# Kernel tuning notes

Hardware: AMD Instinct MI355X
Metric: run time of the kernel (lower is better)

## Reference

```python
import jax, jax.numpy as jnp
import numpy as np

N_NODES = 50000
N_EDGES = 800000
N_GRAPHS = 512
IN_CH = 64
HID = 64
NEG_SLOPE = 0.2  # PyG GATConv default


def leaky_relu(x):
    return jnp.where(x >= 0, x, NEG_SLOPE * x)


def gat_conv(x, src, dst, W, a_src, a_dst, bias):
    # x: [N, in]; src/dst: [E] (self-loops already included)
    h = x @ W                                   # [N, hid]
    # per-edge attention logits (heads=1)
    alpha_s = h @ a_src                         # [N]
    alpha_d = h @ a_dst                         # [N]
    logits = leaky_relu(alpha_s[src] + alpha_d[dst])   # [E]
    # segment softmax over destination nodes
    seg_max = jax.ops.segment_max(logits, dst, num_segments=N_NODES)
    seg_max = jnp.where(jnp.isfinite(seg_max), seg_max, 0.0)
    ex = jnp.exp(logits - seg_max[dst])
    denom = jax.ops.segment_sum(ex, dst, num_segments=N_NODES)
    alpha = ex / jnp.maximum(denom[dst], 1e-16)
    # scatter-weighted aggregation of source features
    out = jax.ops.segment_sum(alpha[:, None] * h[src], dst, num_segments=N_NODES)
    return out + bias


def setup_inputs() -> dict:
    key = jax.random.key(0)
    ks = jax.random.split(key, 12)
    x = jax.random.normal(ks[0], (N_NODES, IN_CH), dtype=jnp.float32)
    edge_index = jax.random.randint(ks[1], (2, N_EDGES), 0, N_NODES, dtype=jnp.int64)
    batch = jnp.sort(jax.random.randint(ks[2], (N_NODES,), 0, N_GRAPHS, dtype=jnp.int64))
    s1 = 1.0 / np.sqrt(IN_CH)
    s2 = 1.0 / np.sqrt(HID)
    W1 = jax.random.normal(ks[3], (IN_CH, HID), dtype=jnp.float32) * s1
    a_src1 = jax.random.normal(ks[4], (HID,), dtype=jnp.float32) * s2
    a_dst1 = jax.random.normal(ks[5], (HID,), dtype=jnp.float32) * s2
    b1 = jnp.zeros((HID,), dtype=jnp.float32)
    W2 = jax.random.normal(ks[6], (HID, HID), dtype=jnp.float32) * s2
    a_src2 = jax.random.normal(ks[7], (HID,), dtype=jnp.float32) * s2
    a_dst2 = jax.random.normal(ks[8], (HID,), dtype=jnp.float32) * s2
    b2 = jnp.zeros((HID,), dtype=jnp.float32)
    return {"x": x, "edge_index": edge_index, "batch": batch,
            "W1": W1, "a_src1": a_src1, "a_dst1": a_dst1, "b1": b1,
            "W2": W2, "a_src2": a_src2, "a_dst2": a_dst2, "b2": b2}


def reference(x, edge_index, batch, W1, a_src1, a_dst1, b1, W2, a_src2, a_dst2, b2):
    # add self-loops (PyG GATConv default add_self_loops=True)
    loops = jnp.arange(N_NODES, dtype=edge_index.dtype)
    src = jnp.concatenate([edge_index[0], loops])
    dst = jnp.concatenate([edge_index[1], loops])
    h = jax.nn.elu(gat_conv(x, src, dst, W1, a_src1, a_dst1, b1))
    h = jax.nn.elu(gat_conv(h, src, dst, W2, a_src2, a_dst2, b2))
    # global mean pool per graph
    sums = jax.ops.segment_sum(h, batch, num_segments=N_GRAPHS)        # [G, hid]
    cnt = jax.ops.segment_sum(jnp.ones((N_NODES,), h.dtype), batch, num_segments=N_GRAPHS)
    return sums / jnp.maximum(cnt, 1.0)[:, None]
```

## Files before the change

### kernel.cpp

```cpp
#include <hip/hip_runtime.h>
#include <hip/hip_bf16.h>
#include <math.h>

#define N_NODES_C 50000
#define N_EDGES_C 800000
#define E_TOT_C   (N_EDGES_C + N_NODES_C)
#define N_GRAPHS_C 512
#define CH 64
#define NBUCK 391
#define NB_BUCK 256
#define BCAP 3328
#define TRF_NODES 64
#define NB_TRF ((N_NODES_C + TRF_NODES - 1) / TRF_NODES)
#define FAT_NODES 32
#define NB_FAT ((N_NODES_C + FAT_NODES - 1) / FAT_NODES)

__device__ __forceinline__ float wave_reduce_sum(float v) {
#pragma unroll
    for (int m = 32; m >= 1; m >>= 1) v += __shfl_xor(v, m, 64);
    return v;
}

__device__ __forceinline__ void fma8(float wv, uint4 u, float* a) {
    a[0] = fmaf(wv, __uint_as_float(u.x << 16), a[0]);
    a[1] = fmaf(wv, __uint_as_float(u.x & 0xFFFF0000u), a[1]);
    a[2] = fmaf(wv, __uint_as_float(u.y << 16), a[2]);
    a[3] = fmaf(wv, __uint_as_float(u.y & 0xFFFF0000u), a[3]);
    a[4] = fmaf(wv, __uint_as_float(u.z << 16), a[4]);
    a[5] = fmaf(wv, __uint_as_float(u.z & 0xFFFF0000u), a[5]);
    a[6] = fmaf(wv, __uint_as_float(u.w << 16), a[6]);
    a[7] = fmaf(wv, __uint_as_float(u.w & 0xFFFF0000u), a[7]);
}


__device__ __forceinline__ float agg_node_value(
    int n, int lane, const __hip_bfloat16* __restrict__ h,
    const float* __restrict__ as, const float* __restrict__ ad,
    const float* __restrict__ bias,
    const unsigned int* __restrict__ row_ptr,
    const unsigned short* __restrict__ csr_src, int& ch_out)
{
    unsigned rp = row_ptr[n];
    float adn = ad[n];
    int beg = (int)(rp >> 8);
    int deg = (int)(rp & 255u);
    int sub = lane >> 3;
    int cg  = (lane & 7) << 3;
    int ch  = cg | sub;
    ch_out = ch;
    if (deg <= 32) {
        int dm = deg - 1;
        int sA = (int)csr_src[beg + min(sub, dm)];
        int sB = (int)csr_src[beg + min(sub + 8, dm)];
        uint4 u0 = *reinterpret_cast<const uint4*>(h + (size_t)sA * CH + cg);
        uint4 u1 = *reinterpret_cast<const uint4*>(h + (size_t)sB * CH + cg);
        bool two = (deg > 16);
        uint4 u2 = make_uint4(0, 0, 0, 0), u3 = make_uint4(0, 0, 0, 0);
        if (two) {
            int sC = (int)csr_src[beg + min(sub + 16, dm)];
            int sD = (int)csr_src[beg + min(sub + 24, dm)];
            u2 = *reinterpret_cast<const uint4*>(h + (size_t)sC * CH + cg);
            u3 = *reinterpret_cast<const uint4*>(h + (size_t)sD * CH + cg);
        }
        int s_reg = (int)csr_src[beg + min(lane, dm)];
        float v0 = as[s_reg] + adn;
        v0 = (v0 >= 0.f) ? v0 : 0.2f * v0;
        float ex = (lane < deg) ? __expf(v0) : 0.f;
        float w0 = __shfl(ex, sub, 64);
        float w1 = __shfl(ex, sub + 8, 64);
        float ssum = wave_reduce_sum(ex);
        float a[8] = {0.f, 0.f, 0.f, 0.f, 0.f, 0.f, 0.f, 0.f};
        fma8(w0, u0, a); fma8(w1, u1, a);
        if (two) {
            float w2 = __shfl(ex, sub + 16, 64);
            float w3 = __shfl(ex, sub + 24, 64);
            fma8(w2, u2, a); fma8(w3, u3, a);
        }
        float inv = 1.f / fmaxf(ssum, 1e-16f);
        bool hi5 = (lane & 32) != 0;
        float t0 = __shfl_xor(hi5 ? a[0] : a[4], 32, 64);
        float t1 = __shfl_xor(hi5 ? a[1] : a[5], 32, 64);
        float t2 = __shfl_xor(hi5 ? a[2] : a[6], 32, 64);
        float t3 = __shfl_xor(hi5 ? a[3] : a[7], 32, 64);
        float b0 = (hi5 ? a[4] : a[0]) + t0;
        float b1 = (hi5 ? a[5] : a[1]) + t1;
        float b2 = (hi5 ? a[6] : a[2]) + t2;
        float b3 = (hi5 ? a[7] : a[3]) + t3;
        bool hi4 = (lane & 16) != 0;
        float u0s = __shfl_xor(hi4 ? b0 : b2, 16, 64);
        float u1s = __shfl_xor(hi4 ? b1 : b3, 16, 64);
        float c0 = (hi4 ? b2 : b0) + u0s;
        float c1 = (hi4 ? b3 : b1) + u1s;
        bool hi3 = (lane & 8) != 0;
        float v1 = __shfl_xor(hi3 ? c0 : c1, 8, 64);
        float r  = (hi3 ? c1 : c0) + v1;
        float v = r * inv + bias[ch];
        return (v > 0.f) ? v : __expf(v) - 1.f;
    } else if (deg <= 64) {
        int s_reg = (int)csr_src[beg + min(lane, deg - 1)];
        float ex = 0.f;
        if (lane < deg) {
            float v = as[s_reg] + adn;
            v = (v >= 0.f) ? v : 0.2f * v;
            ex = __expf(v);
        }
        float ssum = wave_reduce_sum(ex);
        float inv = 1.f / fmaxf(ssum, 1e-16f);
        float a[8] = {0.f, 0.f, 0.f, 0.f, 0.f, 0.f, 0.f, 0.f};
        int full = deg >> 4, rem = deg & 15;
        for (int j = 0; j < full; ++j) {
            int e1 = j * 16 + sub;
            int e2 = e1 + 8;
            int   s1 = __shfl(s_reg, e1, 64);
            int   s2 = __shfl(s_reg, e2, 64);
            float w1 = __shfl(ex, e1, 64);
            float w2 = __shfl(ex, e2, 64);
            uint4 u1 = *reinterpret_cast<const uint4*>(h + (size_t)s1 * CH + cg);
            uint4 u2 = *reinterpret_cast<const uint4*>(h + (size_t)s2 * CH + cg);
            fma8(w1, u1, a); fma8(w2, u2, a);
        }
        if (rem) {
            int dm = deg - 1;
            int e1 = full * 16 + sub;
            int   s1 = __shfl(s_reg, min(e1, dm), 64);
            float w1 = __shfl(ex, e1, 64);
            uint4 u1 = *reinterpret_cast<const uint4*>(h + (size_t)s1 * CH + cg);
            fma8(w1, u1, a);
            if (rem > 8) {
                int e2 = e1 + 8;
                int   s2 = __shfl(s_reg, min(e2, dm), 64);
                float w2 = __shfl(ex, e2, 64);
                uint4 u2 = *reinterpret_cast<const uint4*>(h + (size_t)s2 * CH + cg);
                fma8(w2, u2, a);
            }
        }
        bool hi5 = (lane & 32) != 0;
        float t0 = __shfl_xor(hi5 ? a[0] : a[4], 32, 64);
        float t1 = __shfl_xor(hi5 ? a[1] : a[5], 32, 64);
        float t2 = __shfl_xor(hi5 ? a[2] : a[6], 32, 64);
        float t3 = __shfl_xor(hi5 ? a[3] : a[7], 32, 64);
        float b0 = (hi5 ? a[4] : a[0]) + t0;
        float b1 = (hi5 ? a[5] : a[1]) + t1;
        float b2 = (hi5 ? a[6] : a[2]) + t2;
        float b3 = (hi5 ? a[7] : a[3]) + t3;
        bool hi4 = (lane & 16) != 0;
        float u0s = __shfl_xor(hi4 ? b0 : b2, 16, 64);
        float u1s = __shfl_xor(hi4 ? b1 : b3, 16, 64);
        float c0 = (hi4 ? b2 : b0) + u0s;
        float c1 = (hi4 ? b3 : b1) + u1s;
        bool hi3 = (lane & 8) != 0;
        float v1 = __shfl_xor(hi3 ? c0 : c1, 8, 64);
        float r  = (hi3 ? c1 : c0) + v1;
        float v = r * inv + bias[ch];
        return (v > 0.f) ? v : __expf(v) - 1.f;
    } else {
        ch_out = lane;
        int end = beg + deg;
        float ssum = 0.f;
        for (int i = beg + lane; i < end; i += 64) {
            float v = as[csr_src[i]] + adn;
            v = (v >= 0.f) ? v : 0.2f * v;
            ssum += __expf(v);
        }
        ssum = wave_reduce_sum(ssum);
        float inv = 1.f / fmaxf(ssum, 1e-16f);
        float acc = 0.f;
        for (int i = beg; i < end; ++i) {
            int s = csr_src[i];
            float v = as[s] + adn;
            v = (v >= 0.f) ? v : 0.2f * v;
            float ww = __expf(v);
            acc = fmaf(ww, __bfloat162float(h[(size_t)s * CH + lane]), acc);
        }
        acc = acc * inv + bias[lane];
        return (acc > 0.f) ? acc : __expf(acc) - 1.f;
    }
}


struct __align__(16) TrfSmem {
    __align__(16) float Wl[64][68];
    __align__(16) float xs[64][68];
    float wsv[64], wdv[64];
};
struct BuildSmem { int cnt[NBUCK]; int lbase[NBUCK]; };
union __align__(16) FusedSmem { TrfSmem t; BuildSmem b; };


__device__ __forceinline__ void build_body(
    BuildSmem& sm, int blk, const int* __restrict__ ei,
    int* __restrict__ bucket_cnt, unsigned int* __restrict__ buck_edges)
{
    int t = threadIdx.x;
    for (int i = t; i < NBUCK; i += 256) sm.cnt[i] = 0;
    __syncthreads();
    const int CHUNK = (E_TOT_C + NB_BUCK - 1) / NB_BUCK;
    int beg = blk * CHUNK, end = min(beg + CHUNK, E_TOT_C);
    for (int e = beg + t; e < end; e += 256) {
        int d = (e < N_EDGES_C) ? ei[N_EDGES_C + e] : (e - N_EDGES_C);
        atomicAdd(&sm.cnt[d >> 7], 1);
    }
    __syncthreads();
    for (int b = t; b < NBUCK; b += 256) {
        int c = sm.cnt[b];
        sm.lbase[b] = (c > 0) ? atomicAdd(&bucket_cnt[b], c) : 0;
        sm.cnt[b] = 0;
    }
    __syncthreads();
    for (int e = beg + t; e < end; e += 256) {
        int s_, d_;
        if (e < N_EDGES_C) { s_ = ei[e]; d_ = ei[N_EDGES_C + e]; }
        else               { s_ = d_ = e - N_EDGES_C; }
        int b = d_ >> 7;
        int pos = sm.lbase[b] + atomicAdd(&sm.cnt[b], 1);
        buck_edges[b * BCAP + pos] = ((unsigned)(d_ & 127) << 16) | (unsigned)s_;
    }
}


__device__ __forceinline__ void transform_body(
    TrfSmem& sm, int bb,
    const float* __restrict__ xin, const float* __restrict__ W,
    const float* __restrict__ a_s, const float* __restrict__ a_d,
    __hip_bfloat16* __restrict__ hout, float* __restrict__ as_out,
    float* __restrict__ ad_out)
{
    int t = threadIdx.x;
    const float4* W4 = (const float4*)W;
    for (int i = t; i < 1024; i += 256) {
        int row = i >> 4, f4 = i & 15;
        *reinterpret_cast<float4*>(&sm.Wl[row][f4 * 4]) = W4[i];
    }
    int n0 = bb * TRF_NODES;
    int nn = min(TRF_NODES, N_NODES_C - n0);
    if (nn < TRF_NODES) {
        for (int idx = t; idx < 64 * TRF_NODES; idx += 256) {
            int k = idx >> 6, row = idx & 63;
            if (row >= nn) sm.xs[k][row] = 0.f;
        }
    }
    for (int idx = t; idx < nn * 16; idx += 256) {
        int row = idx >> 4, f4 = idx & 15;
        float4 v = *reinterpret_cast<const float4*>(xin + (size_t)(n0 + row) * CH + f4 * 4);
        sm.xs[f4 * 4 + 0][row] = v.x;
        sm.xs[f4 * 4 + 1][row] = v.y;
        sm.xs[f4 * 4 + 2][row] = v.z;
        sm.xs[f4 * 4 + 3][row] = v.w;
    }
    __syncthreads();
    if (t < 64) {
        float ss = 0.f, dd = 0.f;
#pragma unroll 8
        for (int c2 = 0; c2 < 64; ++c2) {
            float wv = sm.Wl[t][c2];
            ss = fmaf(wv, a_s[c2], ss);
            dd = fmaf(wv, a_d[c2], dd);
        }
        sm.wsv[t] = ss; sm.wdv[t] = dd;
    }
    int w = t >> 6, c = t & 63, lane = t & 63;
    int r0 = w * 16;
    float acc[16];
#pragma unroll
    for (int i = 0; i < 16; ++i) acc[i] = 0.f;
#pragma unroll 8
    for (int k = 0; k < 64; ++k) {
        float wl = sm.Wl[k][c];
        const float4* xp = reinterpret_cast<const float4*>(&sm.xs[k][r0]);
        float4 xa = xp[0], xb = xp[1], xc = xp[2], xd = xp[3];
        acc[0]  = fmaf(xa.x, wl, acc[0]);  acc[1]  = fmaf(xa.y, wl, acc[1]);
        acc[2]  = fmaf(xa.z, wl, acc[2]);  acc[3]  = fmaf(xa.w, wl, acc[3]);
        acc[4]  = fmaf(xb.x, wl, acc[4]);  acc[5]  = fmaf(xb.y, wl, acc[5]);
        acc[6]  = fmaf(xb.z, wl, acc[6]);  acc[7]  = fmaf(xb.w, wl, acc[7]);
        acc[8]  = fmaf(xc.x, wl, acc[8]);  acc[9]  = fmaf(xc.y, wl, acc[9]);
        acc[10] = fmaf(xc.z, wl, acc[10]); acc[11] = fmaf(xc.w, wl, acc[11]);
        acc[12] = fmaf(xd.x, wl, acc[12]); acc[13] = fmaf(xd.y, wl, acc[13]);
        acc[14] = fmaf(xd.z, wl, acc[14]); acc[15] = fmaf(xd.w, wl, acc[15]);
    }
    size_t hb = (size_t)(n0 + r0) * CH + c;
#pragma unroll
    for (int i = 0; i < 16; ++i)
        if (r0 + i < nn) hout[hb + (size_t)i * CH] = __float2bfloat16(acc[i]);
    __syncthreads();
    int kb = lane & 3;
    int rloc = r0 + (lane >> 2);
    float ps = 0.f, pd = 0.f;
#pragma unroll
    for (int j = 0; j < 16; ++j) {
        int k = kb + 4 * j;
        float xv = sm.xs[k][rloc];
        ps = fmaf(xv, sm.wsv[k], ps);
        pd = fmaf(xv, sm.wdv[k], pd);
    }
    ps += __shfl_xor(ps, 1, 64); ps += __shfl_xor(ps, 2, 64);
    pd += __shfl_xor(pd, 1, 64); pd += __shfl_xor(pd, 2, 64);
    if (kb == 0 && rloc < nn) {
        as_out[n0 + rloc] = ps;
        ad_out[n0 + rloc] = pd;
    }
}


__global__ __launch_bounds__(256) void fused_build_trf(
    const int* __restrict__ ei, int* __restrict__ bucket_cnt,
    unsigned int* __restrict__ buck_edges,
    const float* __restrict__ xin, const float* __restrict__ W,
    const float* __restrict__ a_s, const float* __restrict__ a_d,
    __hip_bfloat16* __restrict__ hout, float* __restrict__ as_out,
    float* __restrict__ ad_out)
{
    __shared__ FusedSmem sm;
    if (blockIdx.x < NB_BUCK)
        build_body(sm.b, blockIdx.x, ei, bucket_cnt, buck_edges);
    else
        transform_body(sm.t, blockIdx.x - NB_BUCK, xin, W, a_s, a_d, hout, as_out, ad_out);
}


__global__ __launch_bounds__(512) void bucket_to_csr(const unsigned int* __restrict__ buck_edges,
                                                     const int* __restrict__ bucket_cnt,
                                                     const int* __restrict__ batch,
                                                     unsigned short* __restrict__ csr_src,
                                                     unsigned int* __restrict__ row_ptr,
                                                     int* __restrict__ gstart) {
    __shared__ unsigned int ebuf[BCAP];
    __shared__ unsigned short sbuf[BCAP];
    __shared__ int deg[128], off[128], cur[128];
    __shared__ int wsum;
    int bb = blockIdx.x, t = threadIdx.x;
    if (bb < 196 && t < 256) {
        int i = bb * 256 + t;
        if (i < N_NODES_C) {
            int bcur = batch[i];
            int bprev = (i > 0) ? batch[i - 1] : -1;
            for (int g = bprev + 1; g <= bcur; ++g) gstart[g] = i;
            if (i == N_NODES_C - 1)
                for (int g = bcur + 1; g <= N_GRAPHS_C; ++g) gstart[g] = N_NODES_C;
        }
    }
    int base = bb * BCAP;
    int size = min(bucket_cnt[bb], BCAP);
    int node0 = bb << 7;
    int nnodes = min(128, N_NODES_C - node0);
    for (int i = t; i < size; i += 512) ebuf[i] = buck_edges[base + i];
    if (t < 128) deg[t] = 0;
    __syncthreads();
    for (int i = t; i < size; i += 512) atomicAdd(&deg[(ebuf[i] >> 16) & 127], 1);
    __syncthreads();
    int myscan = 0;
    if (t < 128) {
        int l = t & 63;
        int s = deg[t];
#pragma unroll
        for (int o = 1; o < 64; o <<= 1) {
            int u = __shfl_up(s, o, 64);
            if (l >= o) s += u;
        }
        myscan = s;
        if (t == 63) wsum = s;
    }
    __syncthreads();
    if (t < 128) {
        int add = (t >= 64) ? wsum : 0;
        off[t] = myscan + add - deg[t];
        cur[t] = 0;
    }
    __syncthreads();
    for (int i = t; i < size; i += 512) {
        unsigned pk = ebuf[i];
        int l = (pk >> 16) & 127;
        int p = atomicAdd(&cur[l], 1);
        sbuf[off[l] + p] = (unsigned short)(pk & 0xFFFFu);
    }
    __syncthreads();
    for (int i = t; i < size; i += 512) csr_src[base + i] = sbuf[i];
    if (t < nnodes)
        row_ptr[node0 + t] = ((unsigned)(base + off[t]) << 8) | (unsigned)min(deg[t], 255);
}


struct __align__(16) FatSmem {
    __align__(16) float Wl[64][68];
    __align__(16) float xs[64][36];
    float wsv[64], wdv[64];
};

__global__ __launch_bounds__(512) void fused_agg_trf(
    const __hip_bfloat16* __restrict__ h1, const float* __restrict__ as1n,
    const float* __restrict__ ad1n, const float* __restrict__ b1,
    const unsigned int* __restrict__ row_ptr, const unsigned short* __restrict__ csr_src,
    const float* __restrict__ W2, const float* __restrict__ a_s2,
    const float* __restrict__ a_d2,
    __hip_bfloat16* __restrict__ hout2, float* __restrict__ as_out2,
    float* __restrict__ ad_out2)
{
    __shared__ FatSmem sm;
    int t = threadIdx.x, bb = blockIdx.x;
    int wv = t >> 6, lane = t & 63;
    int n0 = bb * FAT_NODES;
    int nn = min(FAT_NODES, N_NODES_C - n0);
    const float4* W4 = (const float4*)W2;
    for (int i = t; i < 1024; i += 512) {
        int row = i >> 4, f4 = i & 15;
        *reinterpret_cast<float4*>(&sm.Wl[row][f4 * 4]) = W4[i];
    }
    if (nn < FAT_NODES) {
        for (int idx = t; idx < 64 * FAT_NODES; idx += 512) {
            int k = idx >> 5, row = idx & 31;
            if (row >= nn) sm.xs[k][row] = 0.f;
        }
    }
    for (int q = 0; q < 4; ++q) {
        int nl = wv * 4 + q;
        if (nl < nn) {
            int ch;
            float v = agg_node_value(n0 + nl, lane, h1, as1n, ad1n, b1,
                                     row_ptr, csr_src, ch);
            sm.xs[ch][nl] = v;
        }
    }
    __syncthreads();
    if (t < 64) {
        float ss = 0.f, dd = 0.f;
#pragma unroll 8
        for (int c2 = 0; c2 < 64; ++c2) {
            float wv2 = sm.Wl[t][c2];
            ss = fmaf(wv2, a_s2[c2], ss);
            dd = fmaf(wv2, a_d2[c2], dd);
        }
        sm.wsv[t] = ss; sm.wdv[t] = dd;
    }
    int c = lane;
    int r0 = wv * 4;
    float acc[4] = {0.f, 0.f, 0.f, 0.f};
#pragma unroll 8
    for (int k = 0; k < 64; ++k) {
        float wl = sm.Wl[k][c];
        float4 xa = *reinterpret_cast<const float4*>(&sm.xs[k][r0]);
        acc[0] = fmaf(xa.x, wl, acc[0]);
        acc[1] = fmaf(xa.y, wl, acc[1]);
        acc[2] = fmaf(xa.z, wl, acc[2]);
        acc[3] = fmaf(xa.w, wl, acc[3]);
    }
    size_t hb = (size_t)(n0 + r0) * CH + c;
#pragma unroll
    for (int i = 0; i < 4; ++i)
        if (r0 + i < nn) hout2[hb + (size_t)i * CH] = __float2bfloat16(acc[i]);
    __syncthreads();
    int kb = lane & 15;
    int rloc = r0 + (lane >> 4);
    float ps = 0.f, pd = 0.f;
#pragma unroll
    for (int j = 0; j < 4; ++j) {
        int k = kb + 16 * j;
        float xv = sm.xs[k][rloc];
        ps = fmaf(xv, sm.wsv[k], ps);
        pd = fmaf(xv, sm.wdv[k], pd);
    }
    ps += __shfl_xor(ps, 1, 64); ps += __shfl_xor(ps, 2, 64);
    ps += __shfl_xor(ps, 4, 64); ps += __shfl_xor(ps, 8, 64);
    pd += __shfl_xor(pd, 1, 64); pd += __shfl_xor(pd, 2, 64);
    pd += __shfl_xor(pd, 4, 64); pd += __shfl_xor(pd, 8, 64);
    if (kb == 0 && rloc < nn) {
        as_out2[n0 + rloc] = ps;
        ad_out2[n0 + rloc] = pd;
    }
}


__global__ __launch_bounds__(256) void agg_pool(
    const __hip_bfloat16* __restrict__ h2, const float* __restrict__ as2n,
    const float* __restrict__ ad2n, const float* __restrict__ b2,
    const unsigned int* __restrict__ row_ptr, const unsigned short* __restrict__ csr_src,
    const int* __restrict__ batch, const int* __restrict__ gstart,
    float* __restrict__ out)
{
    int t = threadIdx.x;
    int w = t >> 6, lane = t & 63;
    int n = blockIdx.x * 4 + w;
    int ch;
    float v = agg_node_value(n, lane, h2, as2n, ad2n, b2, row_ptr, csr_src, ch);
    int g = batch[n];
    float cnt = (float)(gstart[g + 1] - gstart[g]);
    atomicAdd(&out[g * CH + ch], v / fmaxf(cnt, 1.f));
}


extern "C" void kernel_launch(void* const* d_in, const int* in_sizes, int n_in,
                              void* d_out, int out_size, void* d_ws, size_t ws_size,
                              hipStream_t stream)
{
    const float* x   = (const float*)d_in[0];
    const int*   ei  = (const int*)d_in[1];
    const int*   bat = (const int*)d_in[2];
    const float* W1  = (const float*)d_in[3];
    const float* as1 = (const float*)d_in[4];
    const float* ad1 = (const float*)d_in[5];
    const float* b1  = (const float*)d_in[6];
    const float* W2  = (const float*)d_in[7];
    const float* as2 = (const float*)d_in[8];
    const float* ad2 = (const float*)d_in[9];
    const float* b2  = (const float*)d_in[10];
    float* out = (float*)d_out;

    char* ws = (char*)d_ws;
    size_t off = 0;
    auto alloc = [&](size_t bytes) -> void* {
        void* p = ws + off;
        off += (bytes + 255) & ~size_t(255);
        return p;
    };
    __hip_bfloat16* hbuf1 = (__hip_bfloat16*)alloc(sizeof(__hip_bfloat16) * N_NODES_C * CH);
    __hip_bfloat16* hbuf2 = (__hip_bfloat16*)alloc(sizeof(__hip_bfloat16) * N_NODES_C * CH);
    float* as1n = (float*)alloc(sizeof(float) * N_NODES_C);
    float* ad1n = (float*)alloc(sizeof(float) * N_NODES_C);
    float* as2n = (float*)alloc(sizeof(float) * N_NODES_C);
    float* ad2n = (float*)alloc(sizeof(float) * N_NODES_C);
    int*   bucket_cnt = (int*)alloc(sizeof(int) * NBUCK);
    unsigned int* buck_edges = (unsigned int*)alloc(sizeof(unsigned) * NBUCK * BCAP);
    unsigned short* csr_src  = (unsigned short*)alloc(sizeof(unsigned short) * NBUCK * BCAP);
    unsigned int* row_ptr    = (unsigned int*)alloc(sizeof(unsigned) * N_NODES_C);
    int*   gstart  = (int*)alloc(sizeof(int) * (N_GRAPHS_C + 1));

    const int NB_AGG = N_NODES_C / 4;

    hipMemsetAsync(bucket_cnt, 0, sizeof(int) * NBUCK, stream);
    hipMemsetAsync(out, 0, sizeof(float) * N_GRAPHS_C * CH, stream);

    fused_build_trf<<<NB_BUCK + NB_TRF, 256, 0, stream>>>(ei, bucket_cnt, buck_edges,
                                                          x, W1, as1, ad1,
                                                          hbuf1, as1n, ad1n);
    bucket_to_csr<<<NBUCK, 512, 0, stream>>>(buck_edges, bucket_cnt, bat,
                                             csr_src, row_ptr, gstart);
    fused_agg_trf<<<NB_FAT, 512, 0, stream>>>(hbuf1, as1n, ad1n, b1,
                                              row_ptr, csr_src,
                                              W2, as2, ad2,
                                              hbuf2, as2n, ad2n);
    agg_pool<<<NB_AGG, 256, 0, stream>>>(hbuf2, as2n, ad2n, b2,
                                         row_ptr, csr_src, bat, gstart, out);
}
```

Measured before the change: 180.7 us.

## Precompute per-edge exp attention weights in CSR build and separate edge kernel

Moves the per-edge leaky-relu and exp computation out of the aggregation kernels. Layer-1 weights are now computed in bucket_to_csr, and layer-2 weights in a new edge_weights2 kernel, both stored in edge (CSR) order. The aggregation then reads these contiguous edge weights instead of gathering as[src] and recomputing exp. The cost is an extra kernel launch, an extra per-edge destination-local byte array, and about 3.4 MB of float weights written and read again per layer.

```diff
diff --git a/kernel.cpp b/kernel.cpp
--- a/kernel.cpp
+++ b/kernel.cpp
@@ -35,13 +35,11 @@
 
 __device__ __forceinline__ float agg_node_value(
     int n, int lane, const __hip_bfloat16* __restrict__ h,
-    const float* __restrict__ as, const float* __restrict__ ad,
-    const float* __restrict__ bias,
+    const float* __restrict__ ew, const float* __restrict__ bias,
     const unsigned int* __restrict__ row_ptr,
     const unsigned short* __restrict__ csr_src, int& ch_out)
 {
     unsigned rp = row_ptr[n];
-    float adn = ad[n];
     int beg = (int)(rp >> 8);
     int deg = (int)(rp & 255u);
     int sub = lane >> 3;
@@ -54,28 +52,24 @@
         int sB = (int)csr_src[beg + min(sub + 8, dm)];
         uint4 u0 = *reinterpret_cast<const uint4*>(h + (size_t)sA * CH + cg);
         uint4 u1 = *reinterpret_cast<const uint4*>(h + (size_t)sB * CH + cg);
+        float w0 = (sub     <= dm) ? ew[beg + sub]      : 0.f;
+        float w1 = (sub + 8 <= dm) ? ew[beg + sub + 8]  : 0.f;
+        float ewl = (lane <= dm) ? ew[beg + lane] : 0.f;
         bool two = (deg > 16);
         uint4 u2 = make_uint4(0, 0, 0, 0), u3 = make_uint4(0, 0, 0, 0);
+        float w2 = 0.f, w3 = 0.f;
         if (two) {
             int sC = (int)csr_src[beg + min(sub + 16, dm)];
             int sD = (int)csr_src[beg + min(sub + 24, dm)];
             u2 = *reinterpret_cast<const uint4*>(h + (size_t)sC * CH + cg);
             u3 = *reinterpret_cast<const uint4*>(h + (size_t)sD * CH + cg);
-        }
-        int s_reg = (int)csr_src[beg + min(lane, dm)];
-        float v0 = as[s_reg] + adn;
-        v0 = (v0 >= 0.f) ? v0 : 0.2f * v0;
-        float ex = (lane < deg) ? __expf(v0) : 0.f;
-        float w0 = __shfl(ex, sub, 64);
-        float w1 = __shfl(ex, sub + 8, 64);
-        float ssum = wave_reduce_sum(ex);
+            w2 = (sub + 16 <= dm) ? ew[beg + sub + 16] : 0.f;
+            w3 = (sub + 24 <= dm) ? ew[beg + sub + 24] : 0.f;
+        }
+        float ssum = wave_reduce_sum(ewl);
         float a[8] = {0.f, 0.f, 0.f, 0.f, 0.f, 0.f, 0.f, 0.f};
         fma8(w0, u0, a); fma8(w1, u1, a);
-        if (two) {
-            float w2 = __shfl(ex, sub + 16, 64);
-            float w3 = __shfl(ex, sub + 24, 64);
-            fma8(w2, u2, a); fma8(w3, u3, a);
-        }
+        if (two) { fma8(w2, u2, a); fma8(w3, u3, a); }
         float inv = 1.f / fmaxf(ssum, 1e-16f);
         bool hi5 = (lane & 32) != 0;
         float t0 = __shfl_xor(hi5 ? a[0] : a[4], 32, 64);
@@ -97,39 +91,33 @@
         float v = r * inv + bias[ch];
         return (v > 0.f) ? v : __expf(v) - 1.f;
     } else if (deg <= 64) {
-        int s_reg = (int)csr_src[beg + min(lane, deg - 1)];
-        float ex = 0.f;
-        if (lane < deg) {
-            float v = as[s_reg] + adn;
-            v = (v >= 0.f) ? v : 0.2f * v;
-            ex = __expf(v);
-        }
-        float ssum = wave_reduce_sum(ex);
+        int dm = deg - 1;
+        float ewl = (lane <= dm) ? ew[beg + lane] : 0.f;
+        float ssum = wave_reduce_sum(ewl);
         float inv = 1.f / fmaxf(ssum, 1e-16f);
         float a[8] = {0.f, 0.f, 0.f, 0.f, 0.f, 0.f, 0.f, 0.f};
         int full = deg >> 4, rem = deg & 15;
         for (int j = 0; j < full; ++j) {
             int e1 = j * 16 + sub;
             int e2 = e1 + 8;
-            int   s1 = __shfl(s_reg, e1, 64);
-            int   s2 = __shfl(s_reg, e2, 64);
-            float w1 = __shfl(ex, e1, 64);
-            float w2 = __shfl(ex, e2, 64);
+            int   s1 = (int)csr_src[beg + e1];
+            int   s2 = (int)csr_src[beg + e2];
+            float w1 = ew[beg + e1];
+            float w2 = ew[beg + e2];
             uint4 u1 = *reinterpret_cast<const uint4*>(h + (size_t)s1 * CH + cg);
             uint4 u2 = *reinterpret_cast<const uint4*>(h + (size_t)s2 * CH + cg);
             fma8(w1, u1, a); fma8(w2, u2, a);
         }
         if (rem) {
-            int dm = deg - 1;
             int e1 = full * 16 + sub;
-            int   s1 = __shfl(s_reg, min(e1, dm), 64);
-            float w1 = __shfl(ex, e1, 64);
+            int   s1 = (int)csr_src[beg + min(e1, dm)];
+            float w1 = (e1 <= dm) ? ew[beg + e1] : 0.f;
             uint4 u1 = *reinterpret_cast<const uint4*>(h + (size_t)s1 * CH + cg);
             fma8(w1, u1, a);
             if (rem > 8) {
                 int e2 = e1 + 8;
-                int   s2 = __shfl(s_reg, min(e2, dm), 64);
-                float w2 = __shfl(ex, e2, 64);
+                int   s2 = (int)csr_src[beg + min(e2, dm)];
+                float w2 = (e2 <= dm) ? ew[beg + e2] : 0.f;
                 uint4 u2 = *reinterpret_cast<const uint4*>(h + (size_t)s2 * CH + cg);
                 fma8(w2, u2, a);
             }
@@ -157,20 +145,13 @@
         ch_out = lane;
         int end = beg + deg;
         float ssum = 0.f;
-        for (int i = beg + lane; i < end; i += 64) {
-            float v = as[csr_src[i]] + adn;
-            v = (v >= 0.f) ? v : 0.2f * v;
-            ssum += __expf(v);
-        }
+        for (int i = beg + lane; i < end; i += 64) ssum += ew[i];
         ssum = wave_reduce_sum(ssum);
         float inv = 1.f / fmaxf(ssum, 1e-16f);
         float acc = 0.f;
         for (int i = beg; i < end; ++i) {
-            int s = csr_src[i];
-            float v = as[s] + adn;
-            v = (v >= 0.f) ? v : 0.2f * v;
-            float ww = __expf(v);
-            acc = fmaf(ww, __bfloat162float(h[(size_t)s * CH + lane]), acc);
+            int s = (int)csr_src[i];
+            acc = fmaf(ew[i], __bfloat162float(h[(size_t)s * CH + lane]), acc);
         }
         acc = acc * inv + bias[lane];
         return (acc > 0.f) ? acc : __expf(acc) - 1.f;
@@ -317,14 +298,19 @@
 }
 
 
-__global__ __launch_bounds__(512) void bucket_to_csr(const unsigned int* __restrict__ buck_edges,
-                                                     const int* __restrict__ bucket_cnt,
-                                                     const int* __restrict__ batch,
-                                                     unsigned short* __restrict__ csr_src,
-                                                     unsigned int* __restrict__ row_ptr,
-                                                     int* __restrict__ gstart) {
+__global__ __launch_bounds__(512) void bucket_to_csr(
+    const unsigned int* __restrict__ buck_edges, const int* __restrict__ bucket_cnt,
+    const int* __restrict__ batch,
+    const float* __restrict__ as1, const float* __restrict__ ad1,
+    unsigned short* __restrict__ csr_src, unsigned char* __restrict__ dloc,
+    float* __restrict__ ew, unsigned int* __restrict__ row_ptr,
+    int* __restrict__ gstart)
+{
     __shared__ unsigned int ebuf[BCAP];
     __shared__ unsigned short sbuf[BCAP];
+    __shared__ unsigned char dbuf[BCAP];
+    __shared__ float ewbuf[BCAP];
+    __shared__ float adl[128];
     __shared__ int deg[128], off[128], cur[128];
     __shared__ int wsum;
     int bb = blockIdx.x, t = threadIdx.x;
@@ -343,7 +329,10 @@
     int node0 = bb << 7;
     int nnodes = min(128, N_NODES_C - node0);
     for (int i = t; i < size; i += 512) ebuf[i] = buck_edges[base + i];
-    if (t < 128) deg[t] = 0;
+    if (t < 128) {
+        deg[t] = 0;
+        adl[t] = (t < nnodes) ? ad1[node0 + t] : 0.f;
+    }
     __syncthreads();
     for (int i = t; i < size; i += 512) atomicAdd(&deg[(ebuf[i] >> 16) & 127], 1);
     __syncthreads();
@@ -369,11 +358,21 @@
     for (int i = t; i < size; i += 512) {
         unsigned pk = ebuf[i];
         int l = (pk >> 16) & 127;
+        int s = (int)(pk & 0xFFFFu);
         int p = atomicAdd(&cur[l], 1);
-        sbuf[off[l] + p] = (unsigned short)(pk & 0xFFFFu);
-    }
-    __syncthreads();
-    for (int i = t; i < size; i += 512) csr_src[base + i] = sbuf[i];
+        int slot = off[l] + p;
+        float lg = as1[s] + adl[l];
+        lg = (lg >= 0.f) ? lg : 0.2f * lg;
+        sbuf[slot]  = (unsigned short)s;
+        dbuf[slot]  = (unsigned char)l;
+        ewbuf[slot] = __expf(lg);
+    }
+    __syncthreads();
+    for (int i = t; i < size; i += 512) {
+        csr_src[base + i] = sbuf[i];
+        dloc[base + i]    = dbuf[i];
+        ew[base + i]      = ewbuf[i];
+    }
     if (t < nnodes)
         row_ptr[node0 + t] = ((unsigned)(base + off[t]) << 8) | (unsigned)min(deg[t], 255);
 }
@@ -386,8 +385,8 @@
 };
 
 __global__ __launch_bounds__(512) void fused_agg_trf(
-    const __hip_bfloat16* __restrict__ h1, const float* __restrict__ as1n,
-    const float* __restrict__ ad1n, const float* __restrict__ b1,
+    const __hip_bfloat16* __restrict__ h1, const float* __restrict__ ew,
+    const float* __restrict__ b1,
     const unsigned int* __restrict__ row_ptr, const unsigned short* __restrict__ csr_src,
     const float* __restrict__ W2, const float* __restrict__ a_s2,
     const float* __restrict__ a_d2,
@@ -414,7 +413,7 @@
         int nl = wv * 4 + q;
         if (nl < nn) {
             int ch;
-            float v = agg_node_value(n0 + nl, lane, h1, as1n, ad1n, b1,
+            float v = agg_node_value(n0 + nl, lane, h1, ew, b1,
                                      row_ptr, csr_src, ch);
             sm.xs[ch][nl] = v;
         }
@@ -468,9 +467,33 @@
 }
 
 
+__global__ __launch_bounds__(512) void edge_weights2(
+    const int* __restrict__ bucket_cnt,
+    const unsigned short* __restrict__ csr_src, const unsigned char* __restrict__ dloc,
+    const float* __restrict__ as2, const float* __restrict__ ad2,
+    float* __restrict__ ew)
+{
+    __shared__ float adl[128];
+    int bb = blockIdx.x, t = threadIdx.x;
+    int base = bb * BCAP;
+    int size = min(bucket_cnt[bb], BCAP);
+    int node0 = bb << 7;
+    int nnodes = min(128, N_NODES_C - node0);
+    if (t < 128) adl[t] = (t < nnodes) ? ad2[node0 + t] : 0.f;
+    __syncthreads();
+    for (int i = t; i < size; i += 512) {
+        int s = (int)csr_src[base + i];
+        int l = (int)dloc[base + i];
+        float lg = as2[s] + adl[l];
+        lg = (lg >= 0.f) ? lg : 0.2f * lg;
+        ew[base + i] = __expf(lg);
+    }
+}
+
+
 __global__ __launch_bounds__(256) void agg_pool(
-    const __hip_bfloat16* __restrict__ h2, const float* __restrict__ as2n,
-    const float* __restrict__ ad2n, const float* __restrict__ b2,
+    const __hip_bfloat16* __restrict__ h2, const float* __restrict__ ew,
+    const float* __restrict__ b2,
     const unsigned int* __restrict__ row_ptr, const unsigned short* __restrict__ csr_src,
     const int* __restrict__ batch, const int* __restrict__ gstart,
     float* __restrict__ out)
@@ -479,7 +502,7 @@
     int w = t >> 6, lane = t & 63;
     int n = blockIdx.x * 4 + w;
     int ch;
-    float v = agg_node_value(n, lane, h2, as2n, ad2n, b2, row_ptr, csr_src, ch);
+    float v = agg_node_value(n, lane, h2, ew, b2, row_ptr, csr_src, ch);
     int g = batch[n];
     float cnt = (float)(gstart[g + 1] - gstart[g]);
     atomicAdd(&out[g * CH + ch], v / fmaxf(cnt, 1.f));
@@ -519,6 +542,8 @@
     int*   bucket_cnt = (int*)alloc(sizeof(int) * NBUCK);
     unsigned int* buck_edges = (unsigned int*)alloc(sizeof(unsigned) * NBUCK * BCAP);
     unsigned short* csr_src  = (unsigned short*)alloc(sizeof(unsigned short) * NBUCK * BCAP);
+    unsigned char* dloc      = (unsigned char*)alloc(sizeof(unsigned char) * NBUCK * BCAP);
+    float* ew                = (float*)alloc(sizeof(float) * NBUCK * BCAP);
     unsigned int* row_ptr    = (unsigned int*)alloc(sizeof(unsigned) * N_NODES_C);
     int*   gstart  = (int*)alloc(sizeof(int) * (N_GRAPHS_C + 1));
 
@@ -531,11 +556,14 @@
                                                           x, W1, as1, ad1,
                                                           hbuf1, as1n, ad1n);
     bucket_to_csr<<<NBUCK, 512, 0, stream>>>(buck_edges, bucket_cnt, bat,
-                                             csr_src, row_ptr, gstart);
-    fused_agg_trf<<<NB_FAT, 512, 0, stream>>>(hbuf1, as1n, ad1n, b1,
+                                             as1n, ad1n,
+                                             csr_src, dloc, ew, row_ptr, gstart);
+    fused_agg_trf<<<NB_FAT, 512, 0, stream>>>(hbuf1, ew, b1,
                                               row_ptr, csr_src,
                                               W2, as2, ad2,
                                               hbuf2, as2n, ad2n);
-    agg_pool<<<NB_AGG, 256, 0, stream>>>(hbuf2, as2n, ad2n, b2,
+    edge_weights2<<<NBUCK, 512, 0, stream>>>(bucket_cnt, csr_src, dloc,
+                                             as2n, ad2n, ew);
+    agg_pool<<<NB_AGG, 256, 0, stream>>>(hbuf2, ew, b2,
                                          row_ptr, csr_src, bat, gstart, out);
 }
```

Result: no change. 183.6 us (+1.6%).

## Precompute layer-1 edge weights in CSR build and unfuse agg1 from transform

Applied to the files above, without the earlier changes.

Moves the layer-1 attention logit and exp computation into bucket_to_csr, storing per-edge weights alongside the CSR source indices. The fused aggregate+transform kernel is split into a standalone agg1 kernel that writes fp32 node features, followed by a separate transform kernel. This removes the gathers of as1 and the exp work from the aggregation path and lets agg1 run with small blocks. In exchange it adds an extra kernel launch, a 12.8MB fp32 intermediate write and read, and per-edge weight traffic.

```diff
diff --git a/kernel.cpp b/kernel.cpp
--- a/kernel.cpp
+++ b/kernel.cpp
@@ -12,8 +12,6 @@
 #define BCAP 3328
 #define TRF_NODES 64
 #define NB_TRF ((N_NODES_C + TRF_NODES - 1) / TRF_NODES)
-#define FAT_NODES 32
-#define NB_FAT ((N_NODES_C + FAT_NODES - 1) / FAT_NODES)
 
 __device__ __forceinline__ float wave_reduce_sum(float v) {
 #pragma unroll
@@ -33,7 +31,120 @@
 }
 
 
-__device__ __forceinline__ float agg_node_value(
+__device__ __forceinline__ float tree_reduce_ch(const float* a, int lane) {
+    bool hi5 = (lane & 32) != 0;
+    float t0 = __shfl_xor(hi5 ? a[0] : a[4], 32, 64);
+    float t1 = __shfl_xor(hi5 ? a[1] : a[5], 32, 64);
+    float t2 = __shfl_xor(hi5 ? a[2] : a[6], 32, 64);
+    float t3 = __shfl_xor(hi5 ? a[3] : a[7], 32, 64);
+    float b0 = (hi5 ? a[4] : a[0]) + t0;
+    float b1 = (hi5 ? a[5] : a[1]) + t1;
+    float b2 = (hi5 ? a[6] : a[2]) + t2;
+    float b3 = (hi5 ? a[7] : a[3]) + t3;
+    bool hi4 = (lane & 16) != 0;
+    float u0s = __shfl_xor(hi4 ? b0 : b2, 16, 64);
+    float u1s = __shfl_xor(hi4 ? b1 : b3, 16, 64);
+    float c0 = (hi4 ? b2 : b0) + u0s;
+    float c1 = (hi4 ? b3 : b1) + u1s;
+    bool hi3 = (lane & 8) != 0;
+    float v1 = __shfl_xor(hi3 ? c0 : c1, 8, 64);
+    return (hi3 ? c1 : c0) + v1;
+}
+
+
+__device__ __forceinline__ float agg_node_ew(
+    int n, int lane, const __hip_bfloat16* __restrict__ h,
+    const float* __restrict__ ew, const float* __restrict__ bias,
+    const unsigned int* __restrict__ row_ptr,
+    const unsigned short* __restrict__ csr_src, int& ch_out)
+{
+    unsigned rp = row_ptr[n];
+    int beg = (int)(rp >> 8);
+    int deg = (int)(rp & 255u);
+    int sub = lane >> 3;
+    int cg  = (lane & 7) << 3;
+    int ch  = cg | sub;
+    ch_out = ch;
+    if (deg <= 32) {
+        int dm = deg - 1;
+        int sA = (int)csr_src[beg + min(sub, dm)];
+        int sB = (int)csr_src[beg + min(sub + 8, dm)];
+        uint4 u0 = *reinterpret_cast<const uint4*>(h + (size_t)sA * CH + cg);
+        uint4 u1 = *reinterpret_cast<const uint4*>(h + (size_t)sB * CH + cg);
+        float w0 = (sub     <= dm) ? ew[beg + sub]      : 0.f;
+        float w1 = (sub + 8 <= dm) ? ew[beg + sub + 8]  : 0.f;
+        float ewl = (lane <= dm) ? ew[beg + lane] : 0.f;
+        bool two = (deg > 16);
+        uint4 u2 = make_uint4(0, 0, 0, 0), u3 = make_uint4(0, 0, 0, 0);
+        float w2 = 0.f, w3 = 0.f;
+        if (two) {
+            int sC = (int)csr_src[beg + min(sub + 16, dm)];
+            int sD = (int)csr_src[beg + min(sub + 24, dm)];
+            u2 = *reinterpret_cast<const uint4*>(h + (size_t)sC * CH + cg);
+            u3 = *reinterpret_cast<const uint4*>(h + (size_t)sD * CH + cg);
+            w2 = (sub + 16 <= dm) ? ew[beg + sub + 16] : 0.f;
+            w3 = (sub + 24 <= dm) ? ew[beg + sub + 24] : 0.f;
+        }
+        float ssum = wave_reduce_sum(ewl);
+        float a[8] = {0.f, 0.f, 0.f, 0.f, 0.f, 0.f, 0.f, 0.f};
+        fma8(w0, u0, a); fma8(w1, u1, a);
+        if (two) { fma8(w2, u2, a); fma8(w3, u3, a); }
+        float inv = 1.f / fmaxf(ssum, 1e-16f);
+        float r = tree_reduce_ch(a, lane);
+        float v = r * inv + bias[ch];
+        return (v > 0.f) ? v : __expf(v) - 1.f;
+    } else if (deg <= 64) {
+        int dm = deg - 1;
+        float ewl = (lane <= dm) ? ew[beg + lane] : 0.f;
+        float ssum = wave_reduce_sum(ewl);
+        float inv = 1.f / fmaxf(ssum, 1e-16f);
+        float a[8] = {0.f, 0.f, 0.f, 0.f, 0.f, 0.f, 0.f, 0.f};
+        int full = deg >> 4, rem = deg & 15;
+        for (int j = 0; j < full; ++j) {
+            int e1 = j * 16 + sub, e2 = e1 + 8;
+            int   s1 = (int)csr_src[beg + e1];
+            int   s2 = (int)csr_src[beg + e2];
+            float w1 = ew[beg + e1], w2 = ew[beg + e2];
+            uint4 u1 = *reinterpret_cast<const uint4*>(h + (size_t)s1 * CH + cg);
+            uint4 u2 = *reinterpret_cast<const uint4*>(h + (size_t)s2 * CH + cg);
+            fma8(w1, u1, a); fma8(w2, u2, a);
+        }
+        if (rem) {
+            int e1 = full * 16 + sub;
+            int   s1 = (int)csr_src[beg + min(e1, dm)];
+            float w1 = (e1 <= dm) ? ew[beg + e1] : 0.f;
+            uint4 u1 = *reinterpret_cast<const uint4*>(h + (size_t)s1 * CH + cg);
+            fma8(w1, u1, a);
+            if (rem > 8) {
+                int e2 = e1 + 8;
+                int   s2 = (int)csr_src[beg + min(e2, dm)];
+                float w2 = (e2 <= dm) ? ew[beg + e2] : 0.f;
+                uint4 u2 = *reinterpret_cast<const uint4*>(h + (size_t)s2 * CH + cg);
+                fma8(w2, u2, a);
+            }
+        }
+        float r = tree_reduce_ch(a, lane);
+        float v = r * inv + bias[ch];
+        return (v > 0.f) ? v : __expf(v) - 1.f;
+    } else {
+        ch_out = lane;
+        int end = beg + deg;
+        float ssum = 0.f;
+        for (int i = beg + lane; i < end; i += 64) ssum += ew[i];
+        ssum = wave_reduce_sum(ssum);
+        float inv = 1.f / fmaxf(ssum, 1e-16f);
+        float acc = 0.f;
+        for (int i = beg; i < end; ++i) {
+            int s = (int)csr_src[i];
+            acc = fmaf(ew[i], __bfloat162float(h[(size_t)s * CH + lane]), acc);
+        }
+        acc = acc * inv + bias[lane];
+        return (acc > 0.f) ? acc : __expf(acc) - 1.f;
+    }
+}
+
+
+__device__ __forceinline__ float agg_node_asad(
     int n, int lane, const __hip_bfloat16* __restrict__ h,
     const float* __restrict__ as, const float* __restrict__ ad,
     const float* __restrict__ bias,
@@ -77,23 +188,7 @@
             fma8(w2, u2, a); fma8(w3, u3, a);
         }
         float inv = 1.f / fmaxf(ssum, 1e-16f);
-        bool hi5 = (lane & 32) != 0;
-        float t0 = __shfl_xor(hi5 ? a[0] : a[4], 32, 64);
-        float t1 = __shfl_xor(hi5 ? a[1] : a[5], 32, 64);
-        float t2 = __shfl_xor(hi5 ? a[2] : a[6], 32, 64);
-        float t3 = __shfl_xor(hi5 ? a[3] : a[7], 32, 64);
-        float b0 = (hi5 ? a[4] : a[0]) + t0;
-        float b1 = (hi5 ? a[5] : a[1]) + t1;
-        float b2 = (hi5 ? a[6] : a[2]) + t2;
-        float b3 = (hi5 ? a[7] : a[3]) + t3;
-        bool hi4 = (lane & 16) != 0;
-        float u0s = __shfl_xor(hi4 ? b0 : b2, 16, 64);
-        float u1s = __shfl_xor(hi4 ? b1 : b3, 16, 64);
-        float c0 = (hi4 ? b2 : b0) + u0s;
-        float c1 = (hi4 ? b3 : b1) + u1s;
-        bool hi3 = (lane & 8) != 0;
-        float v1 = __shfl_xor(hi3 ? c0 : c1, 8, 64);
-        float r  = (hi3 ? c1 : c0) + v1;
+        float r = tree_reduce_ch(a, lane);
         float v = r * inv + bias[ch];
         return (v > 0.f) ? v : __expf(v) - 1.f;
     } else if (deg <= 64) {
@@ -109,8 +204,7 @@
         float a[8] = {0.f, 0.f, 0.f, 0.f, 0.f, 0.f, 0.f, 0.f};
         int full = deg >> 4, rem = deg & 15;
         for (int j = 0; j < full; ++j) {
-            int e1 = j * 16 + sub;
-            int e2 = e1 + 8;
+            int e1 = j * 16 + sub, e2 = e1 + 8;
             int   s1 = __shfl(s_reg, e1, 64);
             int   s2 = __shfl(s_reg, e2, 64);
             float w1 = __shfl(ex, e1, 64);
@@ -134,23 +228,7 @@
                 fma8(w2, u2, a);
             }
         }
-        bool hi5 = (lane & 32) != 0;
-        float t0 = __shfl_xor(hi5 ? a[0] : a[4], 32, 64);
-        float t1 = __shfl_xor(hi5 ? a[1] : a[5], 32, 64);
-        float t2 = __shfl_xor(hi5 ? a[2] : a[6], 32, 64);
-        float t3 = __shfl_xor(hi5 ? a[3] : a[7], 32, 64);
-        float b0 = (hi5 ? a[4] : a[0]) + t0;
-        float b1 = (hi5 ? a[5] : a[1]) + t1;
-        float b2 = (hi5 ? a[6] : a[2]) + t2;
-        float b3 = (hi5 ? a[7] : a[3]) + t3;
-        bool hi4 = (lane & 16) != 0;
-        float u0s = __shfl_xor(hi4 ? b0 : b2, 16, 64);
-        float u1s = __shfl_xor(hi4 ? b1 : b3, 16, 64);
-        float c0 = (hi4 ? b2 : b0) + u0s;
-        float c1 = (hi4 ? b3 : b1) + u1s;
-        bool hi3 = (lane & 8) != 0;
-        float v1 = __shfl_xor(hi3 ? c0 : c1, 8, 64);
-        float r  = (hi3 ? c1 : c0) + v1;
+        float r = tree_reduce_ch(a, lane);
         float v = r * inv + bias[ch];
         return (v > 0.f) ? v : __expf(v) - 1.f;
     } else {
@@ -316,15 +394,28 @@
         transform_body(sm.t, blockIdx.x - NB_BUCK, xin, W, a_s, a_d, hout, as_out, ad_out);
 }
 
-
-__global__ __launch_bounds__(512) void bucket_to_csr(const unsigned int* __restrict__ buck_edges,
-                                                     const int* __restrict__ bucket_cnt,
-                                                     const int* __restrict__ batch,
-                                                     unsigned short* __restrict__ csr_src,
-                                                     unsigned int* __restrict__ row_ptr,
-                                                     int* __restrict__ gstart) {
+__global__ __launch_bounds__(256) void transform_kernel(
+    const float* __restrict__ xin, const float* __restrict__ W,
+    const float* __restrict__ a_s, const float* __restrict__ a_d,
+    __hip_bfloat16* __restrict__ hout, float* __restrict__ as_out,
+    float* __restrict__ ad_out)
+{
+    __shared__ TrfSmem sm;
+    transform_body(sm, blockIdx.x, xin, W, a_s, a_d, hout, as_out, ad_out);
+}
+
+
+__global__ __launch_bounds__(512) void bucket_to_csr(
+    const unsigned int* __restrict__ buck_edges, const int* __restrict__ bucket_cnt,
+    const int* __restrict__ batch,
+    const float* __restrict__ as1, const float* __restrict__ ad1,
+    unsigned short* __restrict__ csr_src, float* __restrict__ ew,
+    unsigned int* __restrict__ row_ptr, int* __restrict__ gstart)
+{
     __shared__ unsigned int ebuf[BCAP];
     __shared__ unsigned short sbuf[BCAP];
+    __shared__ float ewbuf[BCAP];
+    __shared__ float adl[128];
     __shared__ int deg[128], off[128], cur[128];
     __shared__ int wsum;
     int bb = blockIdx.x, t = threadIdx.x;
@@ -343,7 +434,10 @@
     int node0 = bb << 7;
     int nnodes = min(128, N_NODES_C - node0);
     for (int i = t; i < size; i += 512) ebuf[i] = buck_edges[base + i];
-    if (t < 128) deg[t] = 0;
+    if (t < 128) {
+        deg[t] = 0;
+        adl[t] = (t < nnodes) ? ad1[node0 + t] : 0.f;
+    }
     __syncthreads();
     for (int i = t; i < size; i += 512) atomicAdd(&deg[(ebuf[i] >> 16) & 127], 1);
     __syncthreads();
@@ -369,106 +463,40 @@
     for (int i = t; i < size; i += 512) {
         unsigned pk = ebuf[i];
         int l = (pk >> 16) & 127;
+        int s = (int)(pk & 0xFFFFu);
         int p = atomicAdd(&cur[l], 1);
-        sbuf[off[l] + p] = (unsigned short)(pk & 0xFFFFu);
-    }
-    __syncthreads();
-    for (int i = t; i < size; i += 512) csr_src[base + i] = sbuf[i];
+        int slot = off[l] + p;
+        float lg = as1[s] + adl[l];
+        lg = (lg >= 0.f) ? lg : 0.2f * lg;
+        sbuf[slot]  = (unsigned short)s;
+        ewbuf[slot] = __expf(lg);
+    }
+    __syncthreads();
+    for (int i = t; i < size; i += 512) {
+        csr_src[base + i] = sbuf[i];
+        ew[base + i]      = ewbuf[i];
+    }
     if (t < nnodes)
         row_ptr[node0 + t] = ((unsigned)(base + off[t]) << 8) | (unsigned)min(deg[t], 255);
 }
 
 
-struct __align__(16) FatSmem {
-    __align__(16) float Wl[64][68];
-    __align__(16) float xs[64][36];
-    float wsv[64], wdv[64];
-};
-
-__global__ __launch_bounds__(512) void fused_agg_trf(
-    const __hip_bfloat16* __restrict__ h1, const float* __restrict__ as1n,
-    const float* __restrict__ ad1n, const float* __restrict__ b1,
+__global__ __launch_bounds__(256) void agg1_kernel(
+    const __hip_bfloat16* __restrict__ h1, const float* __restrict__ ew,
+    const float* __restrict__ b1,
     const unsigned int* __restrict__ row_ptr, const unsigned short* __restrict__ csr_src,
-    const float* __restrict__ W2, const float* __restrict__ a_s2,
-    const float* __restrict__ a_d2,
-    __hip_bfloat16* __restrict__ hout2, float* __restrict__ as_out2,
-    float* __restrict__ ad_out2)
-{
-    __shared__ FatSmem sm;
-    int t = threadIdx.x, bb = blockIdx.x;
-    int wv = t >> 6, lane = t & 63;
-    int n0 = bb * FAT_NODES;
-    int nn = min(FAT_NODES, N_NODES_C - n0);
-    const float4* W4 = (const float4*)W2;
-    for (int i = t; i < 1024; i += 512) {
-        int row = i >> 4, f4 = i & 15;
-        *reinterpret_cast<float4*>(&sm.Wl[row][f4 * 4]) = W4[i];
-    }
-    if (nn < FAT_NODES) {
-        for (int idx = t; idx < 64 * FAT_NODES; idx += 512) {
-            int k = idx >> 5, row = idx & 31;
-            if (row >= nn) sm.xs[k][row] = 0.f;
-        }
-    }
-    for (int q = 0; q < 4; ++q) {
-        int nl = wv * 4 + q;
-        if (nl < nn) {
-            int ch;
-            float v = agg_node_value(n0 + nl, lane, h1, as1n, ad1n, b1,
-                                     row_ptr, csr_src, ch);
-            sm.xs[ch][nl] = v;
-        }
-    }
-    __syncthreads();
-    if (t < 64) {
-        float ss = 0.f, dd = 0.f;
-#pragma unroll 8
-        for (int c2 = 0; c2 < 64; ++c2) {
-            float wv2 = sm.Wl[t][c2];
-            ss = fmaf(wv2, a_s2[c2], ss);
-            dd = fmaf(wv2, a_d2[c2], dd);
-        }
-        sm.wsv[t] = ss; sm.wdv[t] = dd;
-    }
-    int c = lane;
-    int r0 = wv * 4;
-    float acc[4] = {0.f, 0.f, 0.f, 0.f};
-#pragma unroll 8
-    for (int k = 0; k < 64; ++k) {
-        float wl = sm.Wl[k][c];
-        float4 xa = *reinterpret_cast<const float4*>(&sm.xs[k][r0]);
-        acc[0] = fmaf(xa.x, wl, acc[0]);
-        acc[1] = fmaf(xa.y, wl, acc[1]);
-        acc[2] = fmaf(xa.z, wl, acc[2]);
-        acc[3] = fmaf(xa.w, wl, acc[3]);
-    }
-    size_t hb = (size_t)(n0 + r0) * CH + c;
-#pragma unroll
-    for (int i = 0; i < 4; ++i)
-        if (r0 + i < nn) hout2[hb + (size_t)i * CH] = __float2bfloat16(acc[i]);
-    __syncthreads();
-    int kb = lane & 15;
-    int rloc = r0 + (lane >> 4);
-    float ps = 0.f, pd = 0.f;
-#pragma unroll
-    for (int j = 0; j < 4; ++j) {
-        int k = kb + 16 * j;
-        float xv = sm.xs[k][rloc];
-        ps = fmaf(xv, sm.wsv[k], ps);
-        pd = fmaf(xv, sm.wdv[k], pd);
-    }
-    ps += __shfl_xor(ps, 1, 64); ps += __shfl_xor(ps, 2, 64);
-    ps += __shfl_xor(ps, 4, 64); ps += __shfl_xor(ps, 8, 64);
-    pd += __shfl_xor(pd, 1, 64); pd += __shfl_xor(pd, 2, 64);
-    pd += __shfl_xor(pd, 4, 64); pd += __shfl_xor(pd, 8, 64);
-    if (kb == 0 && rloc < nn) {
-        as_out2[n0 + rloc] = ps;
-        ad_out2[n0 + rloc] = pd;
-    }
-}
-
-
-__global__ __launch_bounds__(256) void agg_pool(
+    float* __restrict__ out)
+{
+    int t = threadIdx.x;
+    int w = t >> 6, lane = t & 63;
+    int n = blockIdx.x * 4 + w;
+    int ch;
+    float v = agg_node_ew(n, lane, h1, ew, b1, row_ptr, csr_src, ch);
+    out[(size_t)n * CH + ch] = v;
+}
+
+
+__global__ __launch_bounds__(256) void agg2_pool(
     const __hip_bfloat16* __restrict__ h2, const float* __restrict__ as2n,
     const float* __restrict__ ad2n, const float* __restrict__ b2,
     const unsigned int* __restrict__ row_ptr, const unsigned short* __restrict__ csr_src,
@@ -479,7 +507,7 @@
     int w = t >> 6, lane = t & 63;
     int n = blockIdx.x * 4 + w;
     int ch;
-    float v = agg_node_value(n, lane, h2, as2n, ad2n, b2, row_ptr, csr_src, ch);
+    float v = agg_node_asad(n, lane, h2, as2n, ad2n, b2, row_ptr, csr_src, ch);
     int g = batch[n];
     float cnt = (float)(gstart[g + 1] - gstart[g]);
     atomicAdd(&out[g * CH + ch], v / fmaxf(cnt, 1.f));
@@ -512,6 +540,7 @@
     };
     __hip_bfloat16* hbuf1 = (__hip_bfloat16*)alloc(sizeof(__hip_bfloat16) * N_NODES_C * CH);
     __hip_bfloat16* hbuf2 = (__hip_bfloat16*)alloc(sizeof(__hip_bfloat16) * N_NODES_C * CH);
+    float* obuf = (float*)alloc(sizeof(float) * N_NODES_C * CH);
     float* as1n = (float*)alloc(sizeof(float) * N_NODES_C);
     float* ad1n = (float*)alloc(sizeof(float) * N_NODES_C);
     float* as2n = (float*)alloc(sizeof(float) * N_NODES_C);
@@ -519,6 +548,7 @@
     int*   bucket_cnt = (int*)alloc(sizeof(int) * NBUCK);
     unsigned int* buck_edges = (unsigned int*)alloc(sizeof(unsigned) * NBUCK * BCAP);
     unsigned short* csr_src  = (unsigned short*)alloc(sizeof(unsigned short) * NBUCK * BCAP);
+    float* ew                = (float*)alloc(sizeof(float) * NBUCK * BCAP);
     unsigned int* row_ptr    = (unsigned int*)alloc(sizeof(unsigned) * N_NODES_C);
     int*   gstart  = (int*)alloc(sizeof(int) * (N_GRAPHS_C + 1));
 
@@ -531,11 +561,11 @@
                                                           x, W1, as1, ad1,
                                                           hbuf1, as1n, ad1n);
     bucket_to_csr<<<NBUCK, 512, 0, stream>>>(buck_edges, bucket_cnt, bat,
-                                             csr_src, row_ptr, gstart);
-    fused_agg_trf<<<NB_FAT, 512, 0, stream>>>(hbuf1, as1n, ad1n, b1,
-                                              row_ptr, csr_src,
-                                              W2, as2, ad2,
-                                              hbuf2, as2n, ad2n);
-    agg_pool<<<NB_AGG, 256, 0, stream>>>(hbuf2, as2n, ad2n, b2,
-                                         row_ptr, csr_src, bat, gstart, out);
-}
+                                             as1n, ad1n,
+                                             csr_src, ew, row_ptr, gstart);
+    agg1_kernel<<<NB_AGG, 256, 0, stream>>>(hbuf1, ew, b1, row_ptr, csr_src, obuf);
+    transform_kernel<<<NB_TRF, 256, 0, stream>>>(obuf, W2, as2, ad2,
+                                                 hbuf2, as2n, ad2n);
+    agg2_pool<<<NB_AGG, 256, 0, stream>>>(hbuf2, as2n, ad2n, b2,
+                                          row_ptr, csr_src, bat, gstart, out);
+}
```

Result: no change. 182.6 us (+1.0%).
